# Kernel tuning notes

Hardware: AMD Instinct MI355X
Metric: run time of the kernel (lower is better)

The kernel has to match this reference:

```python
import jax, jax.numpy as jnp
import numpy as np

N, E, H, L, R, NG = 8192, 131072, 256, 3, 128, 64
NUM_ELEMENTS = 80
CUTOFF = 12.0
INV_SQRT_2 = 1.0 / np.sqrt(2.0)
INV_SQRT_3 = 1.0 / np.sqrt(3.0)
INV_SQRT_H = 1.0 / np.sqrt(H)


def _glorot(key, shape):
    fan_in, fan_out = shape[-2], shape[-1]
    return jax.random.normal(key, shape, jnp.float32) * np.sqrt(2.0 / (fan_in + fan_out))


def setup_inputs():
    key = jax.random.key(0)
    ks = jax.random.split(key, 24)
    pos = jax.random.normal(ks[0], (N, 3), jnp.float32) * 5.0
    z = jax.random.randint(ks[1], (N,), 0, NUM_ELEMENTS)
    src = jax.random.randint(ks[2], (E,), 0, N)
    off = jax.random.randint(ks[3], (E,), 1, N)
    dst = (src + off) % N  # guarantee no self-loops (dist > 0)
    edge_index = jnp.stack([src, dst])
    batch = jnp.sort(jax.random.randint(ks[4], (N,), 0, NG))
    return {
        "pos": pos,
        "atom_emb": jax.random.normal(ks[5], (NUM_ELEMENTS, H), jnp.float32),
        "ln_w": jnp.ones((L, H), jnp.float32),
        "ln_b": jnp.zeros((L, H), jnp.float32),
        "xp_w1": _glorot(ks[6], (L, H, H)),
        "xp_b1": jnp.zeros((L, H), jnp.float32),
        "xp_w2": _glorot(ks[7], (L, H, 3 * H)),
        "xp_b2": jnp.zeros((L, 3 * H), jnp.float32),
        "rbf_w": _glorot(ks[8], (L, R, 3 * H)),
        "rbf_b": jnp.zeros((L, 3 * H), jnp.float32),
        "vec_w": _glorot(ks[9], (L, H, 2 * H)),
        "xv_w1": _glorot(ks[10], (L, 2 * H, H)),
        "xv_b1": jnp.zeros((L, H), jnp.float32),
        "xv_w2": _glorot(ks[11], (L, H, 3 * H)),
        "xv_b2": jnp.zeros((L, 3 * H), jnp.float32),
        "oe_w1": _glorot(ks[12], (H, H // 2)),
        "oe_b1": jnp.zeros((H // 2,), jnp.float32),
        "oe_w2": _glorot(ks[13], (H // 2, 1)),
        "oe_b2": jnp.zeros((1,), jnp.float32),
        "z": z,
        "edge_index": edge_index,
        "batch": batch,
    }


def _gaussian_rbf(dist):
    offset = jnp.linspace(0.0, CUTOFF, R)
    coeff = -0.5 / (offset[1] - offset[0]) ** 2
    return jnp.exp(coeff * (dist[:, None] - offset[None, :]) ** 2)  # [E, R]


def _layernorm(x, w, b):
    mu = x.mean(-1, keepdims=True)
    var = x.var(-1, keepdims=True)
    return (x - mu) / jnp.sqrt(var + 1e-5) * w + b


def reference(pos, atom_emb, ln_w, ln_b, xp_w1, xp_b1, xp_w2, xp_b2,
              rbf_w, rbf_b, vec_w, xv_w1, xv_b1, xv_w2, xv_b2,
              oe_w1, oe_b1, oe_w2, oe_b2, z, edge_index, batch):
    src, dst = edge_index[0], edge_index[1]
    rel = pos[src] - pos[dst]                       # [E, 3]
    dist = jnp.sqrt((rel ** 2).sum(-1))             # [E]
    edge_rbf = _gaussian_rbf(dist)                  # [E, R]
    edge_vector = rel / dist[:, None]               # [E, 3] unit vectors

    x = atom_emb[z]                                 # [N, H]
    vec = jnp.zeros((N, 3, H), x.dtype)

    for l in range(L):
        # ---- PaiNNMessage ----
        xh = _layernorm(x, ln_w[l], ln_b[l])
        xh = jax.nn.silu(xh @ xp_w1[l] + xp_b1[l]) @ xp_w2[l] + xp_b2[l]  # [N, 3H]
        rbfh = edge_rbf @ rbf_w[l] + rbf_b[l]                             # [E, 3H]
        m = xh[src] * rbfh
        mx, xh2, xh3 = jnp.split(m, 3, axis=-1)
        xh2 = xh2 * INV_SQRT_3
        mvec = (vec[src] * xh2[:, None, :] + xh3[:, None, :] * edge_vector[:, :, None]) * INV_SQRT_H
        dx = jax.ops.segment_sum(mx, dst, num_segments=N)
        dvec = jax.ops.segment_sum(mvec, dst, num_segments=N)
        x = (x + dx) * INV_SQRT_2
        vec = vec + dvec

        # ---- PaiNNUpdate ----
        vp = vec @ vec_w[l]                          # [N, 3, 2H]
        vec1, vec2 = jnp.split(vp, 2, axis=-1)
        vec_dot = (vec1 * vec2).sum(axis=1) * INV_SQRT_H           # [N, H]
        vnorm = jnp.sqrt((vec2 ** 2).sum(axis=1) + 1e-8)           # [N, H]
        h = jnp.concatenate([x, vnorm], axis=-1)
        h = jax.nn.silu(h @ xv_w1[l] + xv_b1[l]) @ xv_w2[l] + xv_b2[l]
        xv1, xv2, xv3 = jnp.split(h, 3, axis=-1)
        dx = (xv1 + xv2 * vec_dot) * INV_SQRT_2
        dvec = xv3[:, None, :] * vec1
        x = (x + dx) * INV_SQRT_2
        vec = vec + dvec

    # ---- energy head: per-atom MLP then per-molecule sum ----
    per_atom = jax.nn.silu(x @ oe_w1 + oe_b1) @ oe_w2 + oe_b2      # [N, 1]
    energy = jax.ops.segment_sum(per_atom, batch, num_segments=NG)  # [NG, 1]
    return energy
```

## Files before the change

### kernel.cpp

```cpp
#include <hip/hip_runtime.h>
#include <hip/hip_bf16.h>
#include <math.h>

#define NN 8192
#define EE 131072
#define HH 256
#define LL 3
#define RR 128
#define NGG 64
#define MSG_WAVES 16

typedef __attribute__((ext_vector_type(8))) short bf16x8;
typedef __attribute__((ext_vector_type(4))) float f32x4;
typedef unsigned short u16;

#if defined(__has_builtin)
#if __has_builtin(__builtin_amdgcn_fdot2_f32_bf16)
#define HAVE_FDOT2 1
typedef __attribute__((ext_vector_type(2))) __bf16 bf16x2_t;
union BU { unsigned u; bf16x2_t v; };
#endif
#if __has_builtin(__builtin_amdgcn_global_load_lds)
#define HAVE_GLL 1
#endif
#endif

union U4 { ushort4 v; unsigned short a[4]; };
union U8 { uint4 v; unsigned short a[8]; unsigned w[4]; };

__device__ __forceinline__ float silu(float v) { return v / (1.0f + expf(-v)); }
__device__ __forceinline__ float b2f(unsigned short u) { return __uint_as_float(((unsigned)u) << 16); }
__device__ __forceinline__ unsigned short f2b(float f) {
    unsigned u = __float_as_uint(f);
    u += 0x7fff + ((u >> 16) & 1);
    return (unsigned short)(u >> 16);
}

constexpr float kInvSqrt2 = 0.70710678118654752440f;
constexpr float kInvSqrt3 = 0.57735026918962576451f;
constexpr float kInvSqrtH = 0.0625f;

__global__ void k_zero(float* __restrict__ p, int n4) {
    int i = blockIdx.x * 256 + threadIdx.x;
    if (i < n4) ((float4*)p)[i] = make_float4(0.f, 0.f, 0.f, 0.f);
}

__global__ __launch_bounds__(256) void k_wt_all(
    const float* __restrict__ xp_w1, const float* __restrict__ xp_w2,
    const float* __restrict__ rbf_w, const float* __restrict__ vec_w,
    const float* __restrict__ xv_w1, const float* __restrict__ xv_w2,
    const float* __restrict__ oe_w1,
    u16* __restrict__ xp_w1T, u16* __restrict__ xp_w2T, u16* __restrict__ rbf_wP,
    u16* __restrict__ vec_wT, u16* __restrict__ xv_w1T, u16* __restrict__ xv_w2T,
    u16* __restrict__ oe_w1T) {
    int bid = blockIdx.x;
    const float* src; u16* dst; int K, N, t, pairmode = 0;
    if (bid < 2400) {
        int l = bid / 800, r = bid % 800;
        if (r < 64)       { src = xp_w1 + (size_t)l * 65536;  dst = xp_w1T + (size_t)l * 65536;  K = 256; N = 256; t = r; }
        else if (r < 256) { src = xp_w2 + (size_t)l * 196608; dst = xp_w2T + (size_t)l * 196608; K = 256; N = 768; t = r - 64; }
        else if (r < 352) { src = rbf_w + (size_t)l * 98304;  dst = rbf_wP + (size_t)l * 98304;  K = 128; N = 768; t = r - 256; pairmode = 1; }
        else if (r < 480) { src = vec_w + (size_t)l * 131072; dst = vec_wT + (size_t)l * 131072; K = 256; N = 512; t = r - 352; }
        else if (r < 608) { src = xv_w1 + (size_t)l * 131072; dst = xv_w1T + (size_t)l * 131072; K = 512; N = 256; t = r - 480; }
        else              { src = xv_w2 + (size_t)l * 196608; dst = xv_w2T + (size_t)l * 196608; K = 256; N = 768; t = r - 608; }
    } else {
        src = oe_w1; dst = oe_w1T; K = 256; N = 128; t = bid - 2400;
    }
    int nx = N >> 5;
    int bn = (t % nx) * 32, bk = (t / nx) * 32;
    int tx = threadIdx.x & 31, ty = threadIdx.x >> 5;
    if (pairmode) {
#pragma unroll
        for (int i = 0; i < 32; i += 8) {
            int k = bk + ty + i, n = bn + tx;
            dst[(size_t)(k >> 1) * 1536 + n * 2 + (k & 1)] = f2b(src[(size_t)k * N + n]);
        }
        return;
    }
    __shared__ float tile[32][33];
#pragma unroll
    for (int i = 0; i < 32; i += 8)
        tile[ty + i][tx] = src[(size_t)(bk + ty + i) * N + bn + tx];
    __syncthreads();
#pragma unroll
    for (int i = 0; i < 32; i += 8)
        dst[(size_t)(bn + ty + i) * K + bk + tx] = f2b(tile[tx][ty + i]);
}

__global__ void k_init_ln(const float* __restrict__ emb, const int* __restrict__ z,
                          const float* __restrict__ w, const float* __restrict__ b,
                          float* __restrict__ x, u16* __restrict__ xlnb) {
    int n = blockIdx.x, t = threadIdx.x;
    float v = emb[z[n] * HH + t];
    x[(size_t)n * HH + t] = v;
    float s = v, q = v * v;
#pragma unroll
    for (int m = 32; m >= 1; m >>= 1) {
        s += __shfl_xor(s, m, 64);
        q += __shfl_xor(q, m, 64);
    }
    __shared__ float s_sum[4], s_sq[4];
    int wid = t >> 6;
    if ((t & 63) == 0) { s_sum[wid] = s; s_sq[wid] = q; }
    __syncthreads();
    float S = s_sum[0] + s_sum[1] + s_sum[2] + s_sum[3];
    float Q = s_sq[0] + s_sq[1] + s_sq[2] + s_sq[3];
    float mu = S * (1.0f / HH);
    float var = Q * (1.0f / HH) - mu * mu;
    float rs = rsqrtf(var + 1e-5f);
    xlnb[(size_t)n * HH + t] = f2b((v - mu) * rs * w[t] + b[t]);
}

__global__ void k_geom_hist(const float* __restrict__ pos, const int* __restrict__ ei,
                            float* __restrict__ ev, int* __restrict__ deg) {
    int e = blockIdx.x * 256 + threadIdx.x;
    if (e >= EE) return;
    int s = ei[e], d = ei[EE + e];
    float rx = pos[s * 3 + 0] - pos[d * 3 + 0];
    float ry = pos[s * 3 + 1] - pos[d * 3 + 1];
    float rz = pos[s * 3 + 2] - pos[d * 3 + 2];
    float dist = sqrtf(rx * rx + ry * ry + rz * rz);
    float inv = 1.0f / dist;
    ((float4*)ev)[e] = make_float4(rx * inv, ry * inv, rz * inv, dist);
    atomicAdd(&deg[d], 1);
}

__global__ void k_scan_sort(const int* __restrict__ deg, int* __restrict__ row_ptr,
                            int* __restrict__ fill, int* __restrict__ dorder) {
    __shared__ int buf[256];
    __shared__ int carry_s;
    int t = threadIdx.x;
    if (t == 0) carry_s = 0;
    __syncthreads();
    for (int r = 0; r < NN; r += 256) {
        int v = deg[r + t];
        buf[t] = v;
        __syncthreads();
        for (int ofs = 1; ofs < 256; ofs <<= 1) {
            int add = (t >= ofs) ? buf[t - ofs] : 0;
            __syncthreads();
            buf[t] += add;
            __syncthreads();
        }
        int excl = buf[t] - v;
        int carry = carry_s;
        row_ptr[r + t] = carry + excl;
        fill[r + t] = carry + excl;
        __syncthreads();
        if (t == 255) carry_s = carry + buf[t];
        __syncthreads();
    }
    if (t == 0) row_ptr[NN] = carry_s;
    __syncthreads();
    __shared__ int bins[256];
    __shared__ int base[256];
    bins[t] = 0;
    __syncthreads();
    for (int d = t; d < NN; d += 256) {
        int b = deg[d]; b = b > 255 ? 255 : b;
        atomicAdd(&bins[b], 1);
    }
    __syncthreads();
    if (t == 0) {
        int acc = 0;
        for (int k = 255; k >= 0; --k) { base[k] = acc; acc += bins[k]; }
    }
    __syncthreads();
    bins[t] = 0;
    __syncthreads();
    for (int d = t; d < NN; d += 256) {
        int b = deg[d]; b = b > 255 ? 255 : b;
        int p = atomicAdd(&bins[b], 1);
        dorder[base[b] + p] = d;
    }
}

__global__ void k_scatter(const int* __restrict__ ei, const float* __restrict__ ev,
                          int* __restrict__ fill, int* __restrict__ srcp,
                          float4* __restrict__ evp, int* __restrict__ kptab,
                          unsigned* __restrict__ gtab) {
    int e = blockIdx.x * 256 + threadIdx.x;
    if (e >= EE) return;
    int d = ei[EE + e];
    int pos = atomicAdd(&fill[d], 1);
    float4 e4 = ((const float4*)ev)[e];
    srcp[pos] = ei[e];
    evp[pos] = e4;
    const float step = 12.0f / 127.0f;
    const float coeff = -0.5f / (step * step);
    float dist = e4.w;
    int k0 = ((int)floorf(dist / step) - 3) & ~1;
    k0 = k0 < 0 ? 0 : (k0 > 120 ? 120 : k0);
    float g[8];
#pragma unroll
    for (int k = 0; k < 8; ++k) {
        float t = dist - (k0 + k) * step;
        g[k] = expf(coeff * t * t);
    }
    kptab[pos] = k0 >> 1;
    unsigned g0 = (unsigned)f2b(g[0]) | ((unsigned)f2b(g[1]) << 16);
    unsigned g1 = (unsigned)f2b(g[2]) | ((unsigned)f2b(g[3]) << 16);
    unsigned g2 = (unsigned)f2b(g[4]) | ((unsigned)f2b(g[5]) << 16);
    unsigned g3 = (unsigned)f2b(g[6]) | ((unsigned)f2b(g[7]) << 16);
    ((uint4*)gtab)[pos] = make_uint4(g0, g1, g2, g3);
}

template <int OUT_BF16, int ACT>
__global__ __launch_bounds__(256) void k_gemm(
    const u16* __restrict__ A, const u16* __restrict__ BT,
    const float* __restrict__ bias, void* __restrict__ C, int M, int K, int N) {
    __shared__ u16 As[64 * 64];
    __shared__ u16 Bs[128 * 64];
    int tid = threadIdx.x;
    int wave = tid >> 6, lane = tid & 63;
    int bm = blockIdx.y * 64, bn = blockIdx.x * 128;
    int wm = (wave & 1) * 32, wn = (wave >> 1) * 64;
    int lm = lane & 15;
    int kg = lane >> 4;
    f32x4 acc[2][4] = {};

    for (int k0 = 0; k0 < K; k0 += 64) {
#pragma unroll
        for (int it = 0; it < 2; ++it) {
            int idx = it * 256 + tid;
            int r = idx >> 3, seg = idx & 7;
#ifdef HAVE_GLL
            __builtin_amdgcn_global_load_lds(
                (const unsigned*)&A[(size_t)(bm + r) * K + k0 + seg * 8],
                (unsigned*)&As[idx * 8], 16, 0, 0);
#else
            *(uint4*)&As[idx * 8] = *(const uint4*)&A[(size_t)(bm + r) * K + k0 + seg * 8];
#endif
        }
#pragma unroll
        for (int it = 0; it < 4; ++it) {
            int idx = it * 256 + tid;
            int r = idx >> 3, seg = idx & 7;
#ifdef HAVE_GLL
            __builtin_amdgcn_global_load_lds(
                (const unsigned*)&BT[(size_t)(bn + r) * K + k0 + seg * 8],
                (unsigned*)&Bs[idx * 8], 16, 0, 0);
#else
            *(uint4*)&Bs[idx * 8] = *(const uint4*)&BT[(size_t)(bn + r) * K + k0 + seg * 8];
#endif
        }
        __syncthreads();
#pragma unroll
        for (int kh = 0; kh < 2; ++kh) {
            bf16x8 af[2], bfr[4];
#pragma unroll
            for (int i = 0; i < 2; ++i)
                af[i] = *(const bf16x8*)&As[(wm + i * 16 + lm) * 64 + kh * 32 + kg * 8];
#pragma unroll
            for (int j = 0; j < 4; ++j)
                bfr[j] = *(const bf16x8*)&Bs[(wn + j * 16 + lm) * 64 + kh * 32 + kg * 8];
#pragma unroll
            for (int i = 0; i < 2; ++i)
#pragma unroll
                for (int j = 0; j < 4; ++j)
                    acc[i][j] = __builtin_amdgcn_mfma_f32_16x16x32_bf16(af[i], bfr[j], acc[i][j], 0, 0, 0);
        }
        __syncthreads();
    }

#pragma unroll
    for (int j = 0; j < 4; ++j) {
        int col = bn + wn + j * 16 + lm;
        float bv = bias ? bias[col] : 0.f;
#pragma unroll
        for (int i = 0; i < 2; ++i) {
            int row0 = bm + wm + i * 16 + kg * 4;
#pragma unroll
            for (int r = 0; r < 4; ++r) {
                float v = acc[i][j][r] + bv;
                if (ACT) v = silu(v);
                if (OUT_BF16)
                    ((u16*)C)[(size_t)(row0 + r) * N + col] = f2b(v);
                else
                    ((float*)C)[(size_t)(row0 + r) * N + col] = v;
            }
        }
    }
}

__global__ __launch_bounds__(1024) void k_msg(
    const u16* __restrict__ xhb, const u16* __restrict__ vinb,
    const int* __restrict__ srcp, const float4* __restrict__ evp,
    const int* __restrict__ row_ptr, const int* __restrict__ kptab,
    const unsigned* __restrict__ gtab, const u16* __restrict__ WP ,
    const float* __restrict__ rbias, float* __restrict__ x,
    const float* __restrict__ vin, u16* __restrict__ vecMb,
    const int* __restrict__ dorder) {
    __shared__ u16 Wp[64 * 512];
    int tid = threadIdx.x;
    int wave = tid >> 6, lane = tid & 63;
    int c0 = lane * 4;
    int d = dorder[blockIdx.x * MSG_WAVES + wave];
    int E0 = row_ptr[d], E1 = row_ptr[d + 1];
    float accv[3][4] = {};

#pragma unroll
    for (int p = 0; p < 3; ++p) {
        __syncthreads();
#pragma unroll
        for (int it = 0; it < 4; ++it) {
            int idx = it * 1024 + tid;
            int r = idx >> 6;
            int c8 = (idx & 63) * 8;
            *(uint4*)&Wp[r * 512 + c8] =
                *(const uint4*)&WP[(size_t)r * 1536 + p * 512 + c8];
        }
        __syncthreads();
        float4 bb = ((const float4*)(rbias + p * 256))[lane];
        float bias4[4] = {bb.x, bb.y, bb.z, bb.w};
        float accx[4] = {};
        for (int j = E0; j < E1; ++j) {
            int s = srcp[j];
            int kp = kptab[j];
            uint4 gt = ((const uint4*)gtab)[j];
            unsigned gp[4] = {gt.x, gt.y, gt.z, gt.w};
            float rr[4] = {bias4[0], bias4[1], bias4[2], bias4[3]};
#pragma unroll
            for (int p2 = 0; p2 < 4; ++p2) {
                U8 w;
                w.v = *(const uint4*)&Wp[(kp + p2) * 512 + c0 * 2];
#ifdef HAVE_FDOT2
                BU gv; gv.u = gp[p2];
#pragma unroll
                for (int c = 0; c < 4; ++c) {
                    BU wv; wv.u = w.w[c];
                    rr[c] = __builtin_amdgcn_fdot2_f32_bf16(wv.v, gv.v, rr[c], false);
                }
#else
                float ge = b2f((u16)(gp[p2] & 0xffff));
                float go = b2f((u16)(gp[p2] >> 16));
#pragma unroll
                for (int c = 0; c < 4; ++c)
                    rr[c] += ge * b2f(w.a[2 * c]) + go * b2f(w.a[2 * c + 1]);
#endif
            }
            if (p == 0) {
                U4 X; X.v = *(const ushort4*)(xhb + (size_t)s * 768 + c0);
#pragma unroll
                for (int c = 0; c < 4; ++c) accx[c] += b2f(X.a[c]) * rr[c];
            } else if (p == 1) {
                U4 X, V0, V1, V2;
                X.v = *(const ushort4*)(xhb + (size_t)s * 768 + 256 + c0);
                V0.v = *(const ushort4*)(vinb + (size_t)s * 768 + c0);
                V1.v = *(const ushort4*)(vinb + (size_t)s * 768 + 256 + c0);
                V2.v = *(const ushort4*)(vinb + (size_t)s * 768 + 512 + c0);
#pragma unroll
                for (int c = 0; c < 4; ++c) {
                    float m1 = b2f(X.a[c]) * rr[c] * kInvSqrt3;
                    accv[0][c] += b2f(V0.a[c]) * m1;
                    accv[1][c] += b2f(V1.a[c]) * m1;
                    accv[2][c] += b2f(V2.a[c]) * m1;
                }
            } else {
                U4 X; X.v = *(const ushort4*)(xhb + (size_t)s * 768 + 512 + c0);
                float4 ev4 = evp[j];
#pragma unroll
                for (int c = 0; c < 4; ++c) {
                    float m2 = b2f(X.a[c]) * rr[c];
                    accv[0][c] += m2 * ev4.x;
                    accv[1][c] += m2 * ev4.y;
                    accv[2][c] += m2 * ev4.z;
                }
            }
        }
        if (p == 0) {
            size_t xi = (size_t)d * 256 + c0;
            float4 xv = *(const float4*)&x[xi];
            xv.x = (xv.x + accx[0]) * kInvSqrt2;
            xv.y = (xv.y + accx[1]) * kInvSqrt2;
            xv.z = (xv.z + accx[2]) * kInvSqrt2;
            xv.w = (xv.w + accx[3]) * kInvSqrt2;
            *(float4*)&x[xi] = xv;
        }
    }
#pragma unroll
    for (int k = 0; k < 3; ++k) {
        size_t idx = (size_t)d * 768 + k * 256 + c0;
        float4 vv = *(const float4*)&vin[idx];
        ushort4 u;
        u.x = f2b(vv.x + accv[k][0] * kInvSqrtH);
        u.y = f2b(vv.y + accv[k][1] * kInvSqrtH);
        u.z = f2b(vv.z + accv[k][2] * kInvSqrtH);
        u.w = f2b(vv.w + accv[k][3] * kInvSqrtH);
        *(ushort4*)&vecMb[idx] = u;
    }
}

__global__ void k_vecdot(const u16* __restrict__ vp, const float* __restrict__ x,
                         float* __restrict__ vec_dot, u16* __restrict__ hcat) {
    int i = blockIdx.x * 256 + threadIdx.x;
    int n = i >> 8, c = i & 255;
    const u16* p = vp + (size_t)n * 1536;
    float dsum = 0.f, qsum = 0.f;
#pragma unroll
    for (int k = 0; k < 3; ++k) {
        float v1 = b2f(p[k * 512 + c]);
        float v2 = b2f(p[k * 512 + 256 + c]);
        dsum += v1 * v2;
        qsum += v2 * v2;
    }
    vec_dot[i] = dsum * kInvSqrtH;
    hcat[(size_t)n * 512 + c] = f2b(x[i]);
    hcat[(size_t)n * 512 + 256 + c] = f2b(sqrtf(qsum + 1e-8f));
}

__global__ void k_update_out(const u16* __restrict__ hout, const float* __restrict__ vec_dot,
                             const u16* __restrict__ vp, float* __restrict__ x,
                             const u16* __restrict__ vecMb, float* __restrict__ vfin,
                             u16* __restrict__ vb,
                             const float* __restrict__ lnw, const float* __restrict__ lnb,
                             u16* __restrict__ xout) {
    int n = blockIdx.x, t = threadIdx.x;
    size_t i = (size_t)n * 256 + t;
    float xv1 = b2f(hout[(size_t)n * 768 + t]);
    float xv2 = b2f(hout[(size_t)n * 768 + 256 + t]);
    float xv3 = b2f(hout[(size_t)n * 768 + 512 + t]);
    float dxv = (xv1 + xv2 * vec_dot[i]) * kInvSqrt2;
    float nx = (x[i] + dxv) * kInvSqrt2;
    x[i] = nx;
#pragma unroll
    for (int k = 0; k < 3; ++k) {
        size_t idx = (size_t)n * 768 + k * 256 + t;
        float nv = b2f(vecMb[idx]) + xv3 * b2f(vp[(size_t)n * 1536 + k * 512 + t]);
        vfin[idx] = nv;
        vb[idx] = f2b(nv);
    }
    if (lnw) {
        float s = nx, q = nx * nx;
#pragma unroll
        for (int m = 32; m >= 1; m >>= 1) {
            s += __shfl_xor(s, m, 64);
            q += __shfl_xor(q, m, 64);
        }
        __shared__ float s_sum[4], s_sq[4];
        int wid = t >> 6;
        if ((t & 63) == 0) { s_sum[wid] = s; s_sq[wid] = q; }
        __syncthreads();
        float S = s_sum[0] + s_sum[1] + s_sum[2] + s_sum[3];
        float Q = s_sq[0] + s_sq[1] + s_sq[2] + s_sq[3];
        float mu = S * (1.0f / HH);
        float var = Q * (1.0f / HH) - mu * mu;
        float rs = rsqrtf(var + 1e-5f);
        xout[i] = f2b((nx - mu) * rs * lnw[t] + lnb[t]);
    } else {
        xout[i] = f2b(nx);
    }
}

__global__ void k_energy2(const float* __restrict__ h, const float* __restrict__ w2,
                          const float* __restrict__ b2, const int* __restrict__ batch,
                          float* __restrict__ out) {
    __shared__ float g[NGG];
    int t = threadIdx.x;
    if (t < NGG) g[t] = 0.f;
    __syncthreads();
    int a = blockIdx.x * 256 + t;
    const float4* hr = (const float4*)(h + (size_t)a * 128);
    const float4* w4 = (const float4*)w2;
    float acc = 0.f;
#pragma unroll 8
    for (int i = 0; i < 32; ++i) {
        float4 hv = hr[i], wv = w4[i];
        acc += hv.x * wv.x + hv.y * wv.y + hv.z * wv.z + hv.w * wv.w;
    }
    acc += b2[0];
    atomicAdd(&g[batch[a]], acc);
    __syncthreads();
    if (t < NGG && g[t] != 0.f) atomicAdd(&out[t], g[t]);
}

extern "C" void kernel_launch(void* const* d_in, const int* in_sizes, int n_in,
                              void* d_out, int out_size, void* d_ws, size_t ws_size,
                              hipStream_t stream) {
    const float* pos      = (const float*)d_in[0];
    const float* atom_emb = (const float*)d_in[1];
    const float* ln_w     = (const float*)d_in[2];
    const float* ln_b     = (const float*)d_in[3];
    const float* xp_w1    = (const float*)d_in[4];
    const float* xp_b1    = (const float*)d_in[5];
    const float* xp_w2    = (const float*)d_in[6];
    const float* xp_b2    = (const float*)d_in[7];
    const float* rbf_w    = (const float*)d_in[8];
    const float* rbf_b    = (const float*)d_in[9];
    const float* vec_w    = (const float*)d_in[10];
    const float* xv_w1    = (const float*)d_in[11];
    const float* xv_b1    = (const float*)d_in[12];
    const float* xv_w2    = (const float*)d_in[13];
    const float* xv_b2    = (const float*)d_in[14];
    const float* oe_w1    = (const float*)d_in[15];
    const float* oe_b1    = (const float*)d_in[16];
    const float* oe_w2    = (const float*)d_in[17];
    const float* oe_b2    = (const float*)d_in[18];
    const int*   z        = (const int*)d_in[19];
    const int*   ei       = (const int*)d_in[20];
    const int*   batch    = (const int*)d_in[21];
    float* out = (float*)d_out;

    char* ws = (char*)d_ws;
    size_t off = 0;
    auto alloc = [&](size_t b) {
        void* p = ws + off;
        off = (off + b + 255) & ~(size_t)255;
        return p;
    };
    float*    x      = (float*)alloc((size_t)NN * HH * 4);
    float*    vecA   = (float*)alloc((size_t)NN * 768 * 4);
    u16*      vb     = (u16*)alloc((size_t)NN * 768 * 2);
    u16*      vecMb  = (u16*)alloc((size_t)NN * 768 * 2);
    u16*      xlnb   = (u16*)alloc((size_t)NN * HH * 2);
    u16*      t1b    = (u16*)alloc((size_t)NN * HH * 2);
    u16*      xhb    = (u16*)alloc((size_t)NN * 768 * 2);
    float*    vdot   = (float*)alloc((size_t)NN * HH * 4);
    u16*      vpb    = (u16*)alloc((size_t)NN * 1536 * 2);
    u16*      houtb  = (u16*)alloc((size_t)NN * 768 * 2);
    float*    ev     = (float*)alloc((size_t)EE * 4 * 4);
    int*      deg    = (int*)alloc((size_t)NN * 4);
    int*      row_ptr= (int*)alloc((size_t)(NN + 1) * 4);
    int*      fill   = (int*)alloc((size_t)NN * 4);
    int*      dorder = (int*)alloc((size_t)NN * 4);
    int*      srcp   = (int*)alloc((size_t)EE * 4);
    float4*   evp    = (float4*)alloc((size_t)EE * 16);
    int*      kptab  = (int*)alloc((size_t)EE * 4);
    unsigned* gtab   = (unsigned*)alloc((size_t)EE * 16);
    u16* xp_w1T   = (u16*)alloc((size_t)3 * 256 * 256 * 2);
    u16* xp_w2T   = (u16*)alloc((size_t)3 * 768 * 256 * 2);
    u16* rbf_wP   = (u16*)alloc((size_t)3 * 128 * 768 * 2);
    u16* vec_wT   = (u16*)alloc((size_t)3 * 512 * 256 * 2);
    u16* xv_w1T   = (u16*)alloc((size_t)3 * 256 * 512 * 2);
    u16* xv_w2T   = (u16*)alloc((size_t)3 * 768 * 256 * 2);
    u16* oe_w1T   = (u16*)alloc((size_t)128 * 256 * 2);
    (void)ws_size;

    u16*   h1b   = t1b;
    u16*   hcatb = xhb;
    float* heng  = vdot;
    u16*   xb    = xlnb;

    k_wt_all<<<2432, 256, 0, stream>>>(xp_w1, xp_w2, rbf_w, vec_w, xv_w1, xv_w2, oe_w1,
                                       xp_w1T, xp_w2T, rbf_wP, vec_wT, xv_w1T, xv_w2T, oe_w1T);
    k_zero<<<(36 * 1024 * 1024 / 16 + 255) / 256, 256, 0, stream>>>(vecA, 36 * 1024 * 1024 / 16);
    k_zero<<<8, 256, 0, stream>>>((float*)deg, NN / 4);
    k_init_ln<<<NN, 256, 0, stream>>>(atom_emb, z, ln_w, ln_b, x, xlnb);
    k_geom_hist<<<EE / 256, 256, 0, stream>>>(pos, ei, ev, deg);
    k_scan_sort<<<1, 256, 0, stream>>>(deg, row_ptr, fill, dorder);
    k_scatter<<<EE / 256, 256, 0, stream>>>(ei, ev, fill, srcp, evp, kptab, gtab);

    for (int l = 0; l < LL; ++l) {
        k_gemm<1, 1><<<dim3(2, NN / 64), 256, 0, stream>>>(
            xlnb, xp_w1T + (size_t)l * 256 * 256, xp_b1 + l * HH, t1b, NN, 256, 256);
        k_gemm<1, 0><<<dim3(6, NN / 64), 256, 0, stream>>>(
            t1b, xp_w2T + (size_t)l * 768 * 256, xp_b2 + l * 768, xhb, NN, 256, 768);
        k_msg<<<NN / MSG_WAVES, 1024, 0, stream>>>(
            xhb, vb, srcp, evp, row_ptr, kptab, gtab,
            rbf_wP + (size_t)l * 128 * 768, rbf_b + l * 768, x, vecA, vecMb, dorder);

        k_gemm<1, 0><<<dim3(4, 3 * NN / 64), 256, 0, stream>>>(
            vecMb, vec_wT + (size_t)l * 512 * 256, nullptr, vpb, 3 * NN, 256, 512);
        k_vecdot<<<NN, 256, 0, stream>>>(vpb, x, vdot, hcatb);
        k_gemm<1, 1><<<dim3(2, NN / 64), 256, 0, stream>>>(
            hcatb, xv_w1T + (size_t)l * 256 * 512, xv_b1 + l * HH, h1b, NN, 512, 256);
        k_gemm<1, 0><<<dim3(6, NN / 64), 256, 0, stream>>>(
            h1b, xv_w2T + (size_t)l * 768 * 256, xv_b2 + l * 768, houtb, NN, 256, 768);
        bool last = (l == LL - 1);
        k_update_out<<<NN, 256, 0, stream>>>(
            houtb, vdot, vpb, x, vecMb, vecA, vb,
            last ? nullptr : ln_w + (l + 1) * HH,
            last ? nullptr : ln_b + (l + 1) * HH, xlnb);
    }

    k_gemm<0, 1><<<dim3(1, NN / 64), 256, 0, stream>>>(
        xb, oe_w1T, oe_b1, heng, NN, 256, 128);
    k_zero<<<1, 256, 0, stream>>>(out, NGG / 4);
    k_energy2<<<32, 256, 0, stream>>>(heng, oe_w2, oe_b2, batch, out);
}
```

Baseline: 745.2 us.

## Parallelize CSR scan, prefetch next edge in message loop, narrow GEMM tiles

Splits the single-block degree scan and sort into a three-kernel parallel scan plus a separate sort kernel. In the message kernel, the next edge's source index, RBF table entries and gathered features are loaded one iteration ahead (software prefetch), and the four-term RBF dot product is fully unrolled. The GEMM is templated on the N-tile width so the N=256 and N=128 GEMMs use 64-wide tiles and launch more blocks. This trades extra registers and kernel launches for more memory-level parallelism and better GPU occupancy.

```diff
diff --git a/kernel.cpp b/kernel.cpp
--- a/kernel.cpp
+++ b/kernel.cpp
@@ -125,35 +125,42 @@
     atomicAdd(&deg[d], 1);
 }
 
-__global__ void k_scan_sort(const int* __restrict__ deg, int* __restrict__ row_ptr,
-                            int* __restrict__ fill, int* __restrict__ dorder) {
+__global__ void k_scan1(const int* __restrict__ deg, int* __restrict__ row_ptr,
+                        int* __restrict__ csum) {
     __shared__ int buf[256];
-    __shared__ int carry_s;
-    int t = threadIdx.x;
-    if (t == 0) carry_s = 0;
-    __syncthreads();
-    for (int r = 0; r < NN; r += 256) {
-        int v = deg[r + t];
-        buf[t] = v;
+    int t = threadIdx.x, base = blockIdx.x * 256;
+    int v = deg[base + t];
+    buf[t] = v;
+    __syncthreads();
+    for (int ofs = 1; ofs < 256; ofs <<= 1) {
+        int add = (t >= ofs) ? buf[t - ofs] : 0;
         __syncthreads();
-        for (int ofs = 1; ofs < 256; ofs <<= 1) {
-            int add = (t >= ofs) ? buf[t - ofs] : 0;
-            __syncthreads();
-            buf[t] += add;
-            __syncthreads();
-        }
-        int excl = buf[t] - v;
-        int carry = carry_s;
-        row_ptr[r + t] = carry + excl;
-        fill[r + t] = carry + excl;
+        buf[t] += add;
         __syncthreads();
-        if (t == 255) carry_s = carry + buf[t];
-        __syncthreads();
-    }
-    if (t == 0) row_ptr[NN] = carry_s;
-    __syncthreads();
+    }
+    row_ptr[base + t] = buf[t] - v;
+    if (t == 255) csum[blockIdx.x] = buf[t];
+}
+__global__ void k_scan2(int* __restrict__ csum) {
+    if (threadIdx.x == 0) {
+        int acc = 0;
+        for (int i = 0; i < 32; ++i) { int v = csum[i]; csum[i] = acc; acc += v; }
+        csum[32] = acc;
+    }
+}
+__global__ void k_scan3(const int* __restrict__ csum, int* __restrict__ row_ptr,
+                        int* __restrict__ fill) {
+    int i = blockIdx.x * 256 + threadIdx.x;
+    int v = row_ptr[i] + csum[i >> 8];
+    row_ptr[i] = v;
+    fill[i] = v;
+    if (i == 0) row_ptr[NN] = csum[32];
+}
+
+__global__ void k_sort(const int* __restrict__ deg, int* __restrict__ dorder) {
     __shared__ int bins[256];
     __shared__ int base[256];
+    int t = threadIdx.x;
     bins[t] = 0;
     __syncthreads();
     for (int d = t; d < NN; d += 256) {
@@ -205,19 +212,20 @@
     ((uint4*)gtab)[pos] = make_uint4(g0, g1, g2, g3);
 }
 
-template <int OUT_BF16, int ACT>
+template <int OUT_BF16, int ACT, int TN>
 __global__ __launch_bounds__(256) void k_gemm(
     const u16* __restrict__ A, const u16* __restrict__ BT,
     const float* __restrict__ bias, void* __restrict__ C, int M, int K, int N) {
     __shared__ u16 As[64 * 64];
-    __shared__ u16 Bs[128 * 64];
+    __shared__ u16 Bs[TN * 64];
+    const int NJ = TN / 32;
     int tid = threadIdx.x;
     int wave = tid >> 6, lane = tid & 63;
-    int bm = blockIdx.y * 64, bn = blockIdx.x * 128;
-    int wm = (wave & 1) * 32, wn = (wave >> 1) * 64;
+    int bm = blockIdx.y * 64, bn = blockIdx.x * TN;
+    int wm = (wave & 1) * 32, wn = (wave >> 1) * (TN / 2);
     int lm = lane & 15;
     int kg = lane >> 4;
-    f32x4 acc[2][4] = {};
+    f32x4 acc[2][NJ] = {};
 
     for (int k0 = 0; k0 < K; k0 += 64) {
 #pragma unroll
@@ -233,7 +241,7 @@
 #endif
         }
 #pragma unroll
-        for (int it = 0; it < 4; ++it) {
+        for (int it = 0; it < TN / 32; ++it) {
             int idx = it * 256 + tid;
             int r = idx >> 3, seg = idx & 7;
 #ifdef HAVE_GLL
@@ -247,24 +255,24 @@
         __syncthreads();
 #pragma unroll
         for (int kh = 0; kh < 2; ++kh) {
-            bf16x8 af[2], bfr[4];
+            bf16x8 af[2], bfr[NJ];
 #pragma unroll
             for (int i = 0; i < 2; ++i)
                 af[i] = *(const bf16x8*)&As[(wm + i * 16 + lm) * 64 + kh * 32 + kg * 8];
 #pragma unroll
-            for (int j = 0; j < 4; ++j)
+            for (int j = 0; j < NJ; ++j)
                 bfr[j] = *(const bf16x8*)&Bs[(wn + j * 16 + lm) * 64 + kh * 32 + kg * 8];
 #pragma unroll
             for (int i = 0; i < 2; ++i)
 #pragma unroll
-                for (int j = 0; j < 4; ++j)
+                for (int j = 0; j < NJ; ++j)
                     acc[i][j] = __builtin_amdgcn_mfma_f32_16x16x32_bf16(af[i], bfr[j], acc[i][j], 0, 0, 0);
         }
         __syncthreads();
     }
 
 #pragma unroll
-    for (int j = 0; j < 4; ++j) {
+    for (int j = 0; j < NJ; ++j) {
         int col = bn + wn + j * 16 + lm;
         float bv = bias ? bias[col] : 0.f;
 #pragma unroll
@@ -314,41 +322,81 @@
         float4 bb = ((const float4*)(rbias + p * 256))[lane];
         float bias4[4] = {bb.x, bb.y, bb.z, bb.w};
         float accx[4] = {};
+
+        int kp_n = 0; uint4 gt_n = make_uint4(0, 0, 0, 0);
+        U4 X_n; U4 V0_n, V1_n, V2_n; float4 ev_n;
+        X_n.v = make_ushort4(0, 0, 0, 0);
+        V0_n = X_n; V1_n = X_n; V2_n = X_n;
+        ev_n = make_float4(0.f, 0.f, 0.f, 0.f);
+        if (E0 < E1) {
+            int s0 = srcp[E0];
+            kp_n = kptab[E0];
+            gt_n = ((const uint4*)gtab)[E0];
+            X_n.v = *(const ushort4*)(xhb + (size_t)s0 * 768 + p * 256 + c0);
+            if (p == 1) {
+                V0_n.v = *(const ushort4*)(vinb + (size_t)s0 * 768 + c0);
+                V1_n.v = *(const ushort4*)(vinb + (size_t)s0 * 768 + 256 + c0);
+                V2_n.v = *(const ushort4*)(vinb + (size_t)s0 * 768 + 512 + c0);
+            }
+            if (p == 2) ev_n = evp[E0];
+        }
         for (int j = E0; j < E1; ++j) {
-            int s = srcp[j];
-            int kp = kptab[j];
-            uint4 gt = ((const uint4*)gtab)[j];
-            unsigned gp[4] = {gt.x, gt.y, gt.z, gt.w};
+            int kp = kp_n;
+            uint4 gt = gt_n;
+            U4 X = X_n, V0 = V0_n, V1 = V1_n, V2 = V2_n;
+            float4 ev4 = ev_n;
+            if (j + 1 < E1) {
+                int s2 = srcp[j + 1];
+                kp_n = kptab[j + 1];
+                gt_n = ((const uint4*)gtab)[j + 1];
+                X_n.v = *(const ushort4*)(xhb + (size_t)s2 * 768 + p * 256 + c0);
+                if (p == 1) {
+                    V0_n.v = *(const ushort4*)(vinb + (size_t)s2 * 768 + c0);
+                    V1_n.v = *(const ushort4*)(vinb + (size_t)s2 * 768 + 256 + c0);
+                    V2_n.v = *(const ushort4*)(vinb + (size_t)s2 * 768 + 512 + c0);
+                }
+                if (p == 2) ev_n = evp[j + 1];
+            }
+            unsigned gp0 = gt.x, gp1 = gt.y, gp2 = gt.z, gp3 = gt.w;
             float rr[4] = {bias4[0], bias4[1], bias4[2], bias4[3]};
-#pragma unroll
-            for (int p2 = 0; p2 < 4; ++p2) {
-                U8 w;
-                w.v = *(const uint4*)&Wp[(kp + p2) * 512 + c0 * 2];
+            {
+                U8 w0, w1, w2, w3;
+                w0.v = *(const uint4*)&Wp[(kp + 0) * 512 + c0 * 2];
+                w1.v = *(const uint4*)&Wp[(kp + 1) * 512 + c0 * 2];
+                w2.v = *(const uint4*)&Wp[(kp + 2) * 512 + c0 * 2];
+                w3.v = *(const uint4*)&Wp[(kp + 3) * 512 + c0 * 2];
 #ifdef HAVE_FDOT2
-                BU gv; gv.u = gp[p2];
+                BU g0; g0.u = gp0; BU g1; g1.u = gp1;
+                BU g2; g2.u = gp2; BU g3; g3.u = gp3;
 #pragma unroll
                 for (int c = 0; c < 4; ++c) {
-                    BU wv; wv.u = w.w[c];
-                    rr[c] = __builtin_amdgcn_fdot2_f32_bf16(wv.v, gv.v, rr[c], false);
+                    BU a; a.u = w0.w[c];
+                    rr[c] = __builtin_amdgcn_fdot2_f32_bf16(a.v, g0.v, rr[c], false);
+                    a.u = w1.w[c];
+                    rr[c] = __builtin_amdgcn_fdot2_f32_bf16(a.v, g1.v, rr[c], false);
+                    a.u = w2.w[c];
+                    rr[c] = __builtin_amdgcn_fdot2_f32_bf16(a.v, g2.v, rr[c], false);
+                    a.u = w3.w[c];
+                    rr[c] = __builtin_amdgcn_fdot2_f32_bf16(a.v, g3.v, rr[c], false);
                 }
 #else
-                float ge = b2f((u16)(gp[p2] & 0xffff));
-                float go = b2f((u16)(gp[p2] >> 16));
-#pragma unroll
-                for (int c = 0; c < 4; ++c)
-                    rr[c] += ge * b2f(w.a[2 * c]) + go * b2f(w.a[2 * c + 1]);
+                float ge0 = b2f((u16)(gp0 & 0xffff)), go0 = b2f((u16)(gp0 >> 16));
+                float ge1 = b2f((u16)(gp1 & 0xffff)), go1 = b2f((u16)(gp1 >> 16));
+                float ge2 = b2f((u16)(gp2 & 0xffff)), go2 = b2f((u16)(gp2 >> 16));
+                float ge3 = b2f((u16)(gp3 & 0xffff)), go3 = b2f((u16)(gp3 >> 16));
+#pragma unroll
+                for (int c = 0; c < 4; ++c) {
+                    rr[c] += ge0 * b2f(w0.a[2 * c]) + go0 * b2f(w0.a[2 * c + 1]);
+                    rr[c] += ge1 * b2f(w1.a[2 * c]) + go1 * b2f(w1.a[2 * c + 1]);
+                    rr[c] += ge2 * b2f(w2.a[2 * c]) + go2 * b2f(w2.a[2 * c + 1]);
+                    rr[c] += ge3 * b2f(w3.a[2 * c]) + go3 * b2f(w3.a[2 * c + 1]);
+                }
 #endif
             }
             if (p == 0) {
-                U4 X; X.v = *(const ushort4*)(xhb + (size_t)s * 768 + c0);
 #pragma unroll
                 for (int c = 0; c < 4; ++c) accx[c] += b2f(X.a[c]) * rr[c];
             } else if (p == 1) {
-                U4 X, V0, V1, V2;
-                X.v = *(const ushort4*)(xhb + (size_t)s * 768 + 256 + c0);
-                V0.v = *(const ushort4*)(vinb + (size_t)s * 768 + c0);
-                V1.v = *(const ushort4*)(vinb + (size_t)s * 768 + 256 + c0);
-                V2.v = *(const ushort4*)(vinb + (size_t)s * 768 + 512 + c0);
 #pragma unroll
                 for (int c = 0; c < 4; ++c) {
                     float m1 = b2f(X.a[c]) * rr[c] * kInvSqrt3;
@@ -357,8 +405,6 @@
                     accv[2][c] += b2f(V2.a[c]) * m1;
                 }
             } else {
-                U4 X; X.v = *(const ushort4*)(xhb + (size_t)s * 768 + 512 + c0);
-                float4 ev4 = evp[j];
 #pragma unroll
                 for (int c = 0; c < 4; ++c) {
                     float m2 = b2f(X.a[c]) * rr[c];
@@ -523,6 +569,7 @@
     int*      row_ptr= (int*)alloc((size_t)(NN + 1) * 4);
     int*      fill   = (int*)alloc((size_t)NN * 4);
     int*      dorder = (int*)alloc((size_t)NN * 4);
+    int*      csum   = (int*)alloc((size_t)33 * 4);
     int*      srcp   = (int*)alloc((size_t)EE * 4);
     float4*   evp    = (float4*)alloc((size_t)EE * 16);
     int*      kptab  = (int*)alloc((size_t)EE * 4);
@@ -547,24 +594,27 @@
     k_zero<<<8, 256, 0, stream>>>((float*)deg, NN / 4);
     k_init_ln<<<NN, 256, 0, stream>>>(atom_emb, z, ln_w, ln_b, x, xlnb);
     k_geom_hist<<<EE / 256, 256, 0, stream>>>(pos, ei, ev, deg);
-    k_scan_sort<<<1, 256, 0, stream>>>(deg, row_ptr, fill, dorder);
+    k_scan1<<<32, 256, 0, stream>>>(deg, row_ptr, csum);
+    k_scan2<<<1, 64, 0, stream>>>(csum);
+    k_scan3<<<32, 256, 0, stream>>>(csum, row_ptr, fill);
+    k_sort<<<1, 256, 0, stream>>>(deg, dorder);
     k_scatter<<<EE / 256, 256, 0, stream>>>(ei, ev, fill, srcp, evp, kptab, gtab);
 
     for (int l = 0; l < LL; ++l) {
-        k_gemm<1, 1><<<dim3(2, NN / 64), 256, 0, stream>>>(
+        k_gemm<1, 1, 64><<<dim3(4, NN / 64), 256, 0, stream>>>(
             xlnb, xp_w1T + (size_t)l * 256 * 256, xp_b1 + l * HH, t1b, NN, 256, 256);
-        k_gemm<1, 0><<<dim3(6, NN / 64), 256, 0, stream>>>(
+        k_gemm<1, 0, 128><<<dim3(6, NN / 64), 256, 0, stream>>>(
             t1b, xp_w2T + (size_t)l * 768 * 256, xp_b2 + l * 768, xhb, NN, 256, 768);
         k_msg<<<NN / MSG_WAVES, 1024, 0, stream>>>(
             xhb, vb, srcp, evp, row_ptr, kptab, gtab,
             rbf_wP + (size_t)l * 128 * 768, rbf_b + l * 768, x, vecA, vecMb, dorder);
 
-        k_gemm<1, 0><<<dim3(4, 3 * NN / 64), 256, 0, stream>>>(
+        k_gemm<1, 0, 128><<<dim3(4, 3 * NN / 64), 256, 0, stream>>>(
             vecMb, vec_wT + (size_t)l * 512 * 256, nullptr, vpb, 3 * NN, 256, 512);
         k_vecdot<<<NN, 256, 0, stream>>>(vpb, x, vdot, hcatb);
-        k_gemm<1, 1><<<dim3(2, NN / 64), 256, 0, stream>>>(
+        k_gemm<1, 1, 64><<<dim3(4, NN / 64), 256, 0, stream>>>(
             hcatb, xv_w1T + (size_t)l * 256 * 512, xv_b1 + l * HH, h1b, NN, 512, 256);
-        k_gemm<1, 0><<<dim3(6, NN / 64), 256, 0, stream>>>(
+        k_gemm<1, 0, 128><<<dim3(6, NN / 64), 256, 0, stream>>>(
             h1b, xv_w2T + (size_t)l * 768 * 256, xv_b2 + l * 768, houtb, NN, 256, 768);
         bool last = (l == LL - 1);
         k_update_out<<<NN, 256, 0, stream>>>(
@@ -573,7 +623,7 @@
             last ? nullptr : ln_b + (l + 1) * HH, xlnb);
     }
 
-    k_gemm<0, 1><<<dim3(1, NN / 64), 256, 0, stream>>>(
+    k_gemm<0, 1, 64><<<dim3(2, NN / 64), 256, 0, stream>>>(
         xb, oe_w1T, oe_b1, heng, NN, 256, 128);
     k_zero<<<1, 256, 0, stream>>>(out, NGG / 4);
     k_energy2<<<32, 256, 0, stream>>>(heng, oe_w2, oe_b2, batch, out);
```

Measured after the change: 715.1 us. 1.04x faster.
